# Performance work log

Hardware: AMD Instinct MI355X
Metric: run time of the kernel (lower is better)

The kernel has to match this reference:

```python
import jax, jax.numpy as jnp
import numpy as np

B, H, W = 1024, 28, 28
CLS = 20
POS_FRAC = 0.02
L_COORD, L_OBJ, L_NOOBJ = 5.0, 1.0, 0.5


def setup_inputs() -> dict:
    key = jax.random.key(0)
    k1, k2, k3, k4 = jax.random.split(key, 4)
    pred = jax.random.normal(k1, (B, H, W, 10 + CLS), dtype=jnp.float32)
    resp = (jax.random.uniform(k2, (B, H, W)) < POS_FRAC).astype(jnp.float32)
    boxes = jax.random.uniform(k3, (B, H, W, 8)) * resp[..., None]  # cx,cy,sqrt(w),sqrt(h) x2
    cls = jax.random.uniform(k4, (B, H, W, CLS)) * resp[..., None]
    meta = jnp.concatenate([boxes[..., 0:4], resp[..., None], boxes[..., 4:8], resp[..., None], cls], axis=-1)
    return {"pred": pred, "meta": meta}


def _decode(b):
    # offset2box: (cx, cy, sqrt_w, sqrt_h) -> (x0, y0, x1, y1) with w = sqrt_w^2
    cx, cy = b[..., 0], b[..., 1]
    w, h = b[..., 2] * b[..., 2], b[..., 3] * b[..., 3]
    return jnp.stack([cx - w / 2, cy - h / 2, cx + w / 2, cy + h / 2], axis=-1)


def _iou(a, b):
    x0 = jnp.maximum(a[..., 0], b[..., 0])
    y0 = jnp.maximum(a[..., 1], b[..., 1])
    x1 = jnp.minimum(a[..., 2], b[..., 2])
    y1 = jnp.minimum(a[..., 3], b[..., 3])
    inter = jnp.clip(x1 - x0, 0.0) * jnp.clip(y1 - y0, 0.0)
    area_a = (a[..., 2] - a[..., 0]) * (a[..., 3] - a[..., 1])
    area_b = (b[..., 2] - b[..., 0]) * (b[..., 3] - b[..., 1])
    return inter / (area_a + area_b - inter + 1e-10)


def reference(pred, meta):
    dt = pred.dtype
    # split channels (channels-last; equivalent to the NCHW slicing in the original)
    p_cls = pred[..., 10:]                                       # [B,H,W,CLS]
    t_cls = meta[..., 10:]
    p_resp = jnp.stack([pred[..., 4], pred[..., 9]], axis=-1)    # [B,H,W,2]
    t_resp = jnp.stack([meta[..., 4], meta[..., 9]], axis=-1)
    p_box = jnp.stack([pred[..., 0:4], pred[..., 5:9]], axis=-2)  # [B,H,W,2,4]
    t_box = jnp.stack([meta[..., 0:4], meta[..., 5:9]], axis=-2)

    # positive-cell mask (== top-k gather of cells with summed response > 0.9)
    pos = (t_resp.sum(axis=-1) > 0.9).astype(dt)                 # [B,H,W]

    loss_pos_cls = jnp.sum(pos[..., None] * (p_cls - t_cls) ** 2)

    # IoU matching (constant w.r.t. gradients, as in torch.no_grad)
    iou = jax.lax.stop_gradient(_iou(_decode(t_box), _decode(p_box)))  # [B,H,W,2]
    best = jnp.argmax(iou, axis=-1)                               # [B,H,W]

    p_resp_best = jnp.take_along_axis(p_resp, best[..., None], axis=-1)[..., 0]
    iou_best = jnp.take_along_axis(iou, best[..., None], axis=-1)[..., 0]
    loss_pos_response = jnp.sum(pos * (p_resp_best - iou_best) ** 2)

    p_box_best = jnp.take_along_axis(p_box, best[..., None, None], axis=3)[..., 0, :]
    t_box_best = jnp.take_along_axis(t_box, best[..., None, None], axis=3)[..., 0, :]
    loss_pos_offset = jnp.sum(pos[..., None] * (p_box_best - t_box_best) ** 2)

    # no-object loss over all response slots with label < 1
    neg = (t_resp < 1.0).astype(dt)
    loss_neg_response = jnp.sum(neg * (p_resp - t_resp) ** 2)

    b = pred.shape[0]
    loss_neg_response = loss_neg_response / b * L_NOOBJ
    loss_pos_response = loss_pos_response / b * L_OBJ
    loss_pos_offset = loss_pos_offset / b * L_COORD
    loss_pos_cls = loss_pos_cls / b
    loss_sum = loss_neg_response + loss_pos_response + loss_pos_offset + loss_pos_cls
    return (loss_sum, loss_pos_response, loss_neg_response, loss_pos_cls, loss_pos_offset)
```

## Files before the change

kernel.cpp:

```cpp
#include <hip/hip_runtime.h>

constexpr int   kB      = 1024;
constexpr int   kH      = 28;
constexpr int   kW      = 28;
constexpr int   kCells  = kB * kH * kW;
constexpr int   kCh     = 30;
constexpr int   kCPB    = 256;
constexpr int   kBlocks = kCells / kCPB;
constexpr float kLCoord = 5.0f, kLObj = 1.0f, kLNoobj = 0.5f;

__device__ __forceinline__ float iou_decoded(
    float pcx, float pcy, float psw, float psh,
    float tcx, float tcy, float tsw, float tsh)
{
    float aw = tsw * tsw, ah = tsh * tsh;
    float a0 = tcx - aw * 0.5f, a1 = tcy - ah * 0.5f;
    float a2 = tcx + aw * 0.5f, a3 = tcy + ah * 0.5f;
    float bw = psw * psw, bh = psh * psh;
    float b0 = pcx - bw * 0.5f, b1 = pcy - bh * 0.5f;
    float b2 = pcx + bw * 0.5f, b3 = pcy + bh * 0.5f;
    float x0 = fmaxf(a0, b0), y0 = fmaxf(a1, b1);
    float x1 = fminf(a2, b2), y1 = fminf(a3, b3);
    float inter  = fmaxf(x1 - x0, 0.0f) * fmaxf(y1 - y0, 0.0f);
    float area_a = (a2 - a0) * (a3 - a1);
    float area_b = (b2 - b0) * (b3 - b1);
    return inter / (area_a + area_b - inter + 1e-10f);
}

__global__ __launch_bounds__(256) void yolo_loss_main(
    const float* __restrict__ pred, const float* __restrict__ meta,
    float* __restrict__ ws)
{
    const int t    = threadIdx.x;
    const int cell = blockIdx.x * kCPB + t;

    const float* pc = pred + (size_t)cell * kCh;
    const float* mc = meta + (size_t)cell * kCh;

    float resp = mc[4];
    float p4   = pc[4];
    float p9   = pc[9];

    float l_cls = 0.0f, l_resp = 0.0f, l_off = 0.0f, l_neg = 0.0f;

    if (resp + resp > 0.9f) {
        float pv[kCh], mv[kCh];
        const float2* p2 = reinterpret_cast<const float2*>(pc);
        const float2* m2 = reinterpret_cast<const float2*>(mc);
        #pragma unroll
        for (int i = 0; i < kCh / 2; ++i) {
            float2 a = p2[i]; pv[2 * i] = a.x; pv[2 * i + 1] = a.y;
            float2 b = m2[i]; mv[2 * i] = b.x; mv[2 * i + 1] = b.y;
        }

        const float pos = (mv[4] + mv[9] > 0.9f) ? 1.0f : 0.0f;

        float cls_acc = 0.0f;
        #pragma unroll
        for (int c = 0; c < 20; ++c) {
            float d = pv[10 + c] - mv[10 + c];
            cls_acc += d * d;
        }
        l_cls = pos * cls_acc;

        float iou0 = iou_decoded(pv[0], pv[1], pv[2], pv[3], mv[0], mv[1], mv[2], mv[3]);
        float iou1 = iou_decoded(pv[5], pv[6], pv[7], pv[8], mv[5], mv[6], mv[7], mv[8]);
        bool  best1 = (iou1 > iou0);

        float iou_b    = best1 ? iou1  : iou0;
        float p_resp_b = best1 ? pv[9] : pv[4];
        float dr = p_resp_b - iou_b;
        l_resp = pos * dr * dr;

        float off_acc = 0.0f;
        #pragma unroll
        for (int k = 0; k < 4; ++k) {
            float pb = best1 ? pv[5 + k] : pv[k];
            float tb = best1 ? mv[5 + k] : mv[k];
            float d  = pb - tb;
            off_acc += d * d;
        }
        l_off = pos * off_acc;

        float n0 = (mv[4] < 1.0f) ? 1.0f : 0.0f;
        float n1 = (mv[9] < 1.0f) ? 1.0f : 0.0f;
        float d0 = pv[4] - mv[4], d1 = pv[9] - mv[9];
        l_neg = n0 * d0 * d0 + n1 * d1 * d1;
    } else {
        float n  = (resp < 1.0f) ? 1.0f : 0.0f;
        float d0 = p4 - resp, d1 = p9 - resp;
        l_neg = n * (d0 * d0 + d1 * d1);
    }

    #pragma unroll
    for (int off = 32; off > 0; off >>= 1) {
        l_cls  += __shfl_down(l_cls,  off);
        l_resp += __shfl_down(l_resp, off);
        l_off  += __shfl_down(l_off,  off);
        l_neg  += __shfl_down(l_neg,  off);
    }

    __shared__ float red[4][4];
    const int lane = t & 63;
    const int wid  = t >> 6;
    if (lane == 0) {
        red[0][wid] = l_cls;
        red[1][wid] = l_resp;
        red[2][wid] = l_off;
        red[3][wid] = l_neg;
    }
    __syncthreads();
    if (t == 0) {
        const int b = blockIdx.x;
        ws[0 * kBlocks + b] = red[0][0] + red[0][1] + red[0][2] + red[0][3];
        ws[1 * kBlocks + b] = red[1][0] + red[1][1] + red[1][2] + red[1][3];
        ws[2 * kBlocks + b] = red[2][0] + red[2][1] + red[2][2] + red[2][3];
        ws[3 * kBlocks + b] = red[3][0] + red[3][1] + red[3][2] + red[3][3];
    }
}

__global__ __launch_bounds__(1024) void yolo_loss_reduce(
    const float* __restrict__ ws, float* __restrict__ out)
{
    const int t = threadIdx.x;
    float acc[4] = {0.0f, 0.0f, 0.0f, 0.0f};
    #pragma unroll
    for (int m = 0; m < 4; ++m) {
        for (int i = t; i < kBlocks; i += 1024) {
            acc[m] += ws[m * kBlocks + i];
        }
    }
    #pragma unroll
    for (int off = 32; off > 0; off >>= 1) {
        acc[0] += __shfl_down(acc[0], off);
        acc[1] += __shfl_down(acc[1], off);
        acc[2] += __shfl_down(acc[2], off);
        acc[3] += __shfl_down(acc[3], off);
    }
    __shared__ float red[4][16];
    const int lane = t & 63;
    const int wid  = t >> 6;
    if (lane == 0) {
        red[0][wid] = acc[0];
        red[1][wid] = acc[1];
        red[2][wid] = acc[2];
        red[3][wid] = acc[3];
    }
    __syncthreads();
    if (t == 0) {
        float s[4];
        #pragma unroll
        for (int m = 0; m < 4; ++m) {
            float v = 0.0f;
            #pragma unroll
            for (int w = 0; w < 16; ++w) v += red[m][w];
            s[m] = v;
        }
        float inv_b  = 1.0f / (float)kB;
        float s_cls  = s[0] * inv_b;
        float s_resp = s[1] * inv_b * kLObj;
        float s_off  = s[2] * inv_b * kLCoord;
        float s_neg  = s[3] * inv_b * kLNoobj;
        out[0] = s_neg + s_resp + s_off + s_cls;
        out[1] = s_resp;
        out[2] = s_neg;
        out[3] = s_cls;
        out[4] = s_off;
    }
}

extern "C" void kernel_launch(void* const* d_in, const int* in_sizes, int n_in,
                              void* d_out, int out_size, void* d_ws, size_t ws_size,
                              hipStream_t stream) {
    const float* pred = (const float*)d_in[0];
    const float* meta = (const float*)d_in[1];
    float* out = (float*)d_out;
    float* ws  = (float*)d_ws;

    yolo_loss_main<<<kBlocks, kCPB, 0, stream>>>(pred, meta, ws);
    yolo_loss_reduce<<<1, 1024, 0, stream>>>(ws, out);
}
```

Before: 39.87 us.

## Stream full tiles with coalesced float4 loads for no-object loss, two cells per thread

The kernel now reads each block's 512-cell tile of pred and meta with fully coalesced float4 loads and computes the no-object response loss by tracking each element's channel index. It no longer does strided per-cell reads of channels 4 and 9. Positive-cell work (IoU, offset and class losses) is done in a second pass over two cells per thread, which rereads those cells from cache. This replaces uncoalesced strided access with contiguous streaming, at the cost of reading all channels and extra per-element select logic. Halving the block count also halves the partial sums passed to the reduction kernel.

```diff
diff --git a/kernel.cpp b/kernel.cpp
--- a/kernel.cpp
+++ b/kernel.cpp
@@ -1,12 +1,14 @@
 #include <hip/hip_runtime.h>
 
-constexpr int   kB      = 1024;
-constexpr int   kH      = 28;
-constexpr int   kW      = 28;
-constexpr int   kCells  = kB * kH * kW;
-constexpr int   kCh     = 30;
-constexpr int   kCPB    = 256;
-constexpr int   kBlocks = kCells / kCPB;
+constexpr int   kB       = 1024;
+constexpr int   kH       = 28;
+constexpr int   kW       = 28;
+constexpr int   kCells   = kB * kH * kW;
+constexpr int   kCh      = 30;
+constexpr int   kCellsPB = 512;
+constexpr int   kThreads = 256;
+constexpr int   kBlocks  = kCells / kCellsPB;
+constexpr int   kIters   = kCellsPB * kCh / 4 / kThreads;
 constexpr float kLCoord = 5.0f, kLObj = 1.0f, kLNoobj = 0.5f;
 
 __device__ __forceinline__ float iou_decoded(
@@ -31,65 +33,98 @@
     const float* __restrict__ pred, const float* __restrict__ meta,
     float* __restrict__ ws)
 {
-    const int t    = threadIdx.x;
-    const int cell = blockIdx.x * kCPB + t;
-
-    const float* pc = pred + (size_t)cell * kCh;
-    const float* mc = meta + (size_t)cell * kCh;
-
-    float resp = mc[4];
-    float p4   = pc[4];
-    float p9   = pc[9];
-
-    float l_cls = 0.0f, l_resp = 0.0f, l_off = 0.0f, l_neg = 0.0f;
-
-    if (resp + resp > 0.9f) {
-        float pv[kCh], mv[kCh];
-        const float2* p2 = reinterpret_cast<const float2*>(pc);
-        const float2* m2 = reinterpret_cast<const float2*>(mc);
+    const int t  = threadIdx.x;
+    const int c0 = blockIdx.x * kCellsPB;
+
+    float l_neg = 0.0f;
+    {
+        const size_t fbase = (size_t)c0 * kCh;
+        const float4* p4 = reinterpret_cast<const float4*>(pred + fbase);
+        const float4* m4 = reinterpret_cast<const float4*>(meta + fbase);
+
+        int ch = (4 * t) % 30;
         #pragma unroll
-        for (int i = 0; i < kCh / 2; ++i) {
-            float2 a = p2[i]; pv[2 * i] = a.x; pv[2 * i + 1] = a.y;
-            float2 b = m2[i]; mv[2 * i] = b.x; mv[2 * i + 1] = b.y;
-        }
-
-        const float pos = (mv[4] + mv[9] > 0.9f) ? 1.0f : 0.0f;
-
-        float cls_acc = 0.0f;
-        #pragma unroll
-        for (int c = 0; c < 20; ++c) {
-            float d = pv[10 + c] - mv[10 + c];
-            cls_acc += d * d;
-        }
-        l_cls = pos * cls_acc;
-
-        float iou0 = iou_decoded(pv[0], pv[1], pv[2], pv[3], mv[0], mv[1], mv[2], mv[3]);
-        float iou1 = iou_decoded(pv[5], pv[6], pv[7], pv[8], mv[5], mv[6], mv[7], mv[8]);
-        bool  best1 = (iou1 > iou0);
-
-        float iou_b    = best1 ? iou1  : iou0;
-        float p_resp_b = best1 ? pv[9] : pv[4];
-        float dr = p_resp_b - iou_b;
-        l_resp = pos * dr * dr;
-
-        float off_acc = 0.0f;
-        #pragma unroll
-        for (int k = 0; k < 4; ++k) {
-            float pb = best1 ? pv[5 + k] : pv[k];
-            float tb = best1 ? mv[5 + k] : mv[k];
-            float d  = pb - tb;
-            off_acc += d * d;
-        }
-        l_off = pos * off_acc;
-
-        float n0 = (mv[4] < 1.0f) ? 1.0f : 0.0f;
-        float n1 = (mv[9] < 1.0f) ? 1.0f : 0.0f;
-        float d0 = pv[4] - mv[4], d1 = pv[9] - mv[9];
-        l_neg = n0 * d0 * d0 + n1 * d1 * d1;
-    } else {
-        float n  = (resp < 1.0f) ? 1.0f : 0.0f;
-        float d0 = p4 - resp, d1 = p9 - resp;
-        l_neg = n * (d0 * d0 + d1 * d1);
+        for (int i = 0; i < kIters; ++i) {
+            const int j = t + kThreads * i;
+            float4 p = p4[j];
+            float4 m = m4[j];
+
+            int c = ch;
+            {
+                bool sel = (c == 4) | (c == 9);
+                float d = p.x - m.x;
+                l_neg += (sel && (m.x < 1.0f)) ? d * d : 0.0f;
+            }
+            c++; if (c == 30) c = 0;
+            {
+                bool sel = (c == 4) | (c == 9);
+                float d = p.y - m.y;
+                l_neg += (sel && (m.y < 1.0f)) ? d * d : 0.0f;
+            }
+            c++; if (c == 30) c = 0;
+            {
+                bool sel = (c == 4) | (c == 9);
+                float d = p.z - m.z;
+                l_neg += (sel && (m.z < 1.0f)) ? d * d : 0.0f;
+            }
+            c++; if (c == 30) c = 0;
+            {
+                bool sel = (c == 4) | (c == 9);
+                float d = p.w - m.w;
+                l_neg += (sel && (m.w < 1.0f)) ? d * d : 0.0f;
+            }
+            ch += 4; if (ch >= 30) ch -= 30;
+        }
+    }
+
+    float l_cls = 0.0f, l_resp = 0.0f, l_off = 0.0f;
+    #pragma unroll
+    for (int u = 0; u < 2; ++u) {
+        const int cg = c0 + t + u * kThreads;
+        const float* pc = pred + (size_t)cg * kCh;
+        const float* mc = meta + (size_t)cg * kCh;
+        float resp = mc[4];
+        if (resp + resp > 0.9f) {
+            float pv[10], mv[10];
+            const float2* pp = reinterpret_cast<const float2*>(pc);
+            const float2* mm = reinterpret_cast<const float2*>(mc);
+            #pragma unroll
+            for (int i = 0; i < 5; ++i) {
+                float2 a = pp[i]; pv[2*i] = a.x; pv[2*i+1] = a.y;
+                float2 b = mm[i]; mv[2*i] = b.x; mv[2*i+1] = b.y;
+            }
+            const float pos = (mv[4] + mv[9] > 0.9f) ? 1.0f : 0.0f;
+
+            float iou0 = iou_decoded(pv[0], pv[1], pv[2], pv[3], mv[0], mv[1], mv[2], mv[3]);
+            float iou1 = iou_decoded(pv[5], pv[6], pv[7], pv[8], mv[5], mv[6], mv[7], mv[8]);
+            bool  best1 = (iou1 > iou0);
+
+            float iou_b    = best1 ? iou1  : iou0;
+            float p_resp_b = best1 ? pv[9] : pv[4];
+            float dr = p_resp_b - iou_b;
+            l_resp += pos * dr * dr;
+
+            float off_acc = 0.0f;
+            #pragma unroll
+            for (int k = 0; k < 4; ++k) {
+                float pb = best1 ? pv[5 + k] : pv[k];
+                float tb = best1 ? mv[5 + k] : mv[k];
+                float d  = pb - tb;
+                off_acc += d * d;
+            }
+            l_off += pos * off_acc;
+
+            float cls_acc = 0.0f;
+            const float2* pcl = reinterpret_cast<const float2*>(pc + 10);
+            const float2* mcl = reinterpret_cast<const float2*>(mc + 10);
+            #pragma unroll
+            for (int i = 0; i < 10; ++i) {
+                float2 a = pcl[i], b = mcl[i];
+                float d0 = a.x - b.x, d1 = a.y - b.y;
+                cls_acc += d0 * d0 + d1 * d1;
+            }
+            l_cls += pos * cls_acc;
+        }
     }
 
     #pragma unroll
@@ -177,6 +212,6 @@
     float* out = (float*)d_out;
     float* ws  = (float*)d_ws;
 
-    yolo_loss_main<<<kBlocks, kCPB, 0, stream>>>(pred, meta, ws);
+    yolo_loss_main<<<kBlocks, kThreads, 0, stream>>>(pred, meta, ws);
     yolo_loss_reduce<<<1, 1024, 0, stream>>>(ws, out);
 }
```

Result: slower. 43.56 us (+9.3%).
